# Kernel optimization log

Hardware: AMD Instinct MI355X
Metric: run time of the kernel (lower is better)

The kernel has to match this reference:

```python
import jax, jax.numpy as jnp
import numpy as np

TAU = 0.2        # temperature
LAM = 0.5        # lambda_weight
P = 128          # proj_dim


def l2n(x):
    # tf.math.l2_normalize semantics: x / sqrt(max(sum(x^2), eps))
    return x / jnp.sqrt(jnp.maximum(jnp.sum(x * x, axis=-1, keepdims=True), 1e-12))


def global_head(feat, W1, b1, W2, b2):
    # GlobalAveragePooling2D -> Dense(2048, relu) -> Dense(128); dropout is identity in eval
    g = jnp.mean(feat, axis=(1, 2))                       # [B, C]
    return jax.nn.relu(g @ W1 + b1) @ W2 + b2             # [B, 128]


def dense_head(feat, W1, b1, W2, b2):
    # 1x1 Conv2D(2048, relu) -> 1x1 Conv2D(128) == per-pixel matmuls
    h = jax.nn.relu(jnp.einsum('bhwc,cd->bhwd', feat, W1) + b1)
    return jnp.einsum('bhwd,de->bhwe', h, W2) + b2        # [B, H, W, 128]


def dense_correspondence(q, k):
    b, h, w, c = q.shape
    f1 = q.reshape(b, h * w, c)
    f2 = k.reshape(b, h * w, c)
    sim = jnp.einsum('bnc,bmc->bnm', f1, f2)              # [B, hw, hw]
    idx = jnp.argmax(sim, axis=-1)                        # [B, hw]
    return jnp.take_along_axis(f2, idx[:, :, None], axis=1)  # batched gather


def info_nce(q, k):
    logits = (q @ k.T) / TAU                              # [N, N]
    lse = jax.nn.logsumexp(logits, axis=-1)
    pos = jnp.diagonal(logits)                            # labels = arange(N)
    return jnp.mean(lse - pos)


def queue_info_nce(q, k, queue):
    l_pos = jnp.sum(q * k, axis=-1, keepdims=True)        # [B, 1]
    l_neg = q @ queue.T                                   # [B, Q]
    logits = jnp.concatenate([l_pos, l_neg], axis=1) / TAU
    # labels are all zero -> positive logit is column 0
    return jnp.mean(jax.nn.logsumexp(logits, axis=-1) - logits[:, 0])


def setup_inputs() -> dict:
    key = jax.random.key(0)
    ks = jax.random.split(key, 16)
    B, H, W, C, D = 8, 28, 28, 1024, 2048
    Q = 65536
    s1 = 0.02
    inp = {
        'feat_q': jax.random.normal(ks[0], (B, H, W, C), jnp.float32),
        'feat_k': jax.random.normal(ks[1], (B, H, W, C), jnp.float32),
        'Wg1': jax.random.normal(ks[2], (C, D), jnp.float32) * s1,
        'bg1': jnp.zeros((D,), jnp.float32),
        'Wg2': jax.random.normal(ks[3], (D, P), jnp.float32) * s1,
        'bg2': jnp.zeros((P,), jnp.float32),
        'Wd1': jax.random.normal(ks[4], (C, D), jnp.float32) * s1,
        'bd1': jnp.zeros((D,), jnp.float32),
        'Wd2': jax.random.normal(ks[5], (D, P), jnp.float32) * s1,
        'bd2': jnp.zeros((P,), jnp.float32),
        'mWg1': jax.random.normal(ks[6], (C, D), jnp.float32) * s1,
        'mbg1': jnp.zeros((D,), jnp.float32),
        'mWg2': jax.random.normal(ks[7], (D, P), jnp.float32) * s1,
        'mbg2': jnp.zeros((P,), jnp.float32),
        'mWd1': jax.random.normal(ks[8], (C, D), jnp.float32) * s1,
        'mbd1': jnp.zeros((D,), jnp.float32),
        'mWd2': jax.random.normal(ks[9], (D, P), jnp.float32) * s1,
        'mbd2': jnp.zeros((P,), jnp.float32),
        'queue': l2n(jax.random.normal(ks[10], (Q, P), jnp.float32)),
    }
    return inp


def reference(feat_q, feat_k, Wg1, bg1, Wg2, bg2, Wd1, bd1, Wd2, bd2,
              mWg1, mbg1, mWg2, mbg2, mWd1, mbd1, mWd2, mbd2, queue):
    # student branch
    q_g = l2n(global_head(feat_q, Wg1, bg1, Wg2, bg2))
    q_d = l2n(dense_head(feat_q, Wd1, bd1, Wd2, bd2))
    # momentum (teacher) branch, stop-gradient as in train_step
    k_g = jax.lax.stop_gradient(l2n(global_head(feat_k, mWg1, mbg1, mWg2, mbg2)))
    k_d = jax.lax.stop_gradient(l2n(dense_head(feat_k, mWd1, mbd1, mWd2, mbd2)))
    # post-warmup path (warmup_epochs=0)
    l_g = queue_info_nce(q_g, k_g, queue)
    matched_k = dense_correspondence(q_d, k_d)
    l_d = info_nce(q_d.reshape(-1, P), matched_k.reshape(-1, P))
    total = (1.0 - LAM) * l_g + LAM * l_d
    return total
```

## Files before the change

kernel.cpp:

```cpp
#include <hip/hip_runtime.h>
#include <cstdint>

#define TAU_INV 5.0f
#define L2E 1.4426950408889634f

using ushort = unsigned short;
typedef __attribute__((ext_vector_type(8))) short s16x8;
typedef __attribute__((ext_vector_type(4))) float f32x4;

static __device__ __forceinline__ ushort f2bf(float x) {
  unsigned u = __float_as_uint(x);
  return (ushort)((u + 0x7fffu + ((u >> 16) & 1u)) >> 16);
}

static __device__ __forceinline__ float fexp2(float x) {
#if __has_builtin(__builtin_amdgcn_exp2f)
  return __builtin_amdgcn_exp2f(x);
#else
  return exp2f(x);
#endif
}

static __device__ __forceinline__ void gload_lds16(const void* g, void* l) {
  __builtin_amdgcn_global_load_lds(
      reinterpret_cast<const __attribute__((address_space(1))) void*>(
          reinterpret_cast<uintptr_t>(g)),
      reinterpret_cast<__attribute__((address_space(3))) void*>(
          (unsigned)reinterpret_cast<uintptr_t>(l)),
      16, 0, 0);
}

static __device__ __forceinline__ void xcd_swizzle(int gx, int gy, int& bx, int& by) {
  int nwg = gx * gy;
  int flat = by * gx + bx;
  int q = nwg >> 3, r = nwg & 7;
  int xcd = flat & 7, sl = flat >> 3;
  int tile = (xcd < r ? xcd * (q + 1) : r * (q + 1) + (xcd - r) * q) + sl;
  by = tile / gx;
  bx = tile - by * gx;
}

__global__ void k_prep(const float* __restrict__ fq, const float* __restrict__ fk,
                       ushort* __restrict__ obf, float* __restrict__ gpart,
                       const float* __restrict__ Wd1, const float* __restrict__ mWd1,
                       const float* __restrict__ Wd2, const float* __restrict__ mWd2,
                       ushort* __restrict__ Wt1, ushort* __restrict__ Wt2) {
  int bid = blockIdx.x;
  if (bid < 1792) {
    int pc = bid % 112, yy = bid / 112;
    int br = yy >> 3, b = yy & 7, t = threadIdx.x;
    const float* feat = br ? fk : fq;
    const float* fp = feat + ((size_t)b * 784 + (size_t)pc * 7) * 1024;
    ushort* op = obf + (size_t)br * 6422528 + ((size_t)b * 784 + (size_t)pc * 7) * 1024;
    float4 acc = {0.f, 0.f, 0.f, 0.f};
#pragma unroll
    for (int p = 0; p < 7; ++p) {
      float4 v = ((const float4*)(fp + (size_t)p * 1024))[t];
      acc.x += v.x; acc.y += v.y; acc.z += v.z; acc.w += v.w;
      ushort4 r;
      r.x = f2bf(v.x); r.y = f2bf(v.y); r.z = f2bf(v.z); r.w = f2bf(v.w);
      ((ushort4*)(op + (size_t)p * 1024))[t] = r;
    }
    ((float4*)(gpart + ((size_t)yy * 112 + pc) * 1024))[t] = acc;
  } else {
    int fl2 = bid - 1792;
    int z = fl2 / 2304, fl = fl2 % 2304;
    const float* W;
    ushort* o;
    int bx, by, K, N;
    if (fl < 2048) {
      W = z ? mWd1 : Wd1;
      o = Wt1 + (size_t)z * 2097152;
      bx = fl & 63; by = fl >> 6; K = 1024; N = 2048;
    } else {
      fl -= 2048;
      W = z ? mWd2 : Wd2;
      o = Wt2 + (size_t)z * 262144;
      bx = fl & 3; by = fl >> 2; K = 2048; N = 128;
    }
    __shared__ float tile[32][33];
    int n0 = bx * 32, k0 = by * 32;
    int tx = threadIdx.x & 31, ty = threadIdx.x >> 5;
#pragma unroll
    for (int i = 0; i < 32; i += 8)
      tile[ty + i][tx] = W[(size_t)(k0 + ty + i) * N + n0 + tx];
    __syncthreads();
#pragma unroll
    for (int i = 0; i < 32; i += 8)
      o[(size_t)(n0 + ty + i) * K + k0 + tx] = f2bf(tile[tx][ty + i]);
  }
}

__global__ void k_gpool_fin(const float* __restrict__ gpart, float* __restrict__ g) {
  int idx = blockIdx.x * 256 + threadIdx.x;
  int bb = idx >> 10, c = idx & 1023;
  float s = 0.f;
#pragma unroll 4
  for (int pc = 0; pc < 112; ++pc) s += gpart[((size_t)bb * 112 + pc) * 1024 + c];
  g[idx] = s * (1.0f / 784.0f);
}

__global__ void k_dense1_part(const float* __restrict__ g, const float* __restrict__ W0,
                              const float* __restrict__ W1, float* __restrict__ part1) {
  int br = blockIdx.z;
  const float* gb = g + (size_t)br * 8192;
  const float* W = br ? W1 : W0;
  float* p1 = part1 + (size_t)br * 262144;
  int d = blockIdx.x * 256 + threadIdx.x;
  int k0 = blockIdx.y * 64;
  __shared__ float gs[512];
  for (int i = threadIdx.x; i < 512; i += 256) gs[i] = gb[(i >> 6) * 1024 + k0 + (i & 63)];
  __syncthreads();
  float acc[8] = {};
  for (int kk = 0; kk < 64; ++kk) {
    float w = W[(size_t)(k0 + kk) * 2048 + d];
#pragma unroll
    for (int b = 0; b < 8; ++b) acc[b] += gs[b * 64 + kk] * w;
  }
#pragma unroll
  for (int b = 0; b < 8; ++b) p1[((size_t)blockIdx.y * 8 + b) * 2048 + d] = acc[b];
}

__global__ void k_d12(const float* __restrict__ part1, const float* __restrict__ b10,
                      const float* __restrict__ b11, const float* __restrict__ W20,
                      const float* __restrict__ W21, float* __restrict__ part2) {
  int br = blockIdx.y, k0 = blockIdx.x * 64;
  const float* p1 = part1 + (size_t)br * 262144;
  const float* b1 = br ? b11 : b10;
  const float* W2 = br ? W21 : W20;
  float* p2 = part2 + (size_t)br * 32768;
  __shared__ float hs[512];
  for (int i = threadIdx.x; i < 512; i += 128) {
    int b = i >> 6, kk = i & 63;
    float s = b1[k0 + kk];
#pragma unroll
    for (int ks = 0; ks < 16; ++ks) s += p1[((size_t)ks * 8 + b) * 2048 + k0 + kk];
    hs[i] = fmaxf(s, 0.f);
  }
  __syncthreads();
  int d = threadIdx.x;
  float acc[8] = {};
  for (int kk = 0; kk < 64; ++kk) {
    float w = W2[(size_t)(k0 + kk) * 128 + d];
#pragma unroll
    for (int b = 0; b < 8; ++b) acc[b] += hs[b * 64 + kk] * w;
  }
#pragma unroll
  for (int b = 0; b < 8; ++b) p2[((size_t)blockIdx.x * 8 + b) * 128 + d] = acc[b];
}

__global__ void k_head_fin(const float* __restrict__ p2q, const float* __restrict__ p2k,
                           const float* __restrict__ bq, const float* __restrict__ bk,
                           float* __restrict__ qg, float* __restrict__ kg,
                           float* __restrict__ lpos) {
  int b = blockIdx.x, lane = threadIdx.x;
  float q0 = bq[lane], q1 = bq[lane + 64];
  float k0 = bk[lane], k1 = bk[lane + 64];
#pragma unroll
  for (int s = 0; s < 32; ++s) {
    size_t base = ((size_t)s * 8 + b) * 128;
    q0 += p2q[base + lane]; q1 += p2q[base + lane + 64];
    k0 += p2k[base + lane]; k1 += p2k[base + lane + 64];
  }
  float sq = q0 * q0 + q1 * q1, sk = k0 * k0 + k1 * k1;
#pragma unroll
  for (int d = 1; d < 64; d <<= 1) { sq += __shfl_xor(sq, d); sk += __shfl_xor(sk, d); }
  float rq = 1.0f / sqrtf(fmaxf(sq, 1e-12f));
  float rk = 1.0f / sqrtf(fmaxf(sk, 1e-12f));
  q0 *= rq; q1 *= rq; k0 *= rk; k1 *= rk;
  qg[b * 128 + lane] = q0; qg[b * 128 + 64 + lane] = q1;
  kg[b * 128 + lane] = k0; kg[b * 128 + 64 + lane] = k1;
  float lp = q0 * k0 + q1 * k1;
#pragma unroll
  for (int d = 1; d < 64; d <<= 1) lp += __shfl_xor(lp, d);
  if (lane == 0) lpos[b] = lp;
}

__global__ __launch_bounds__(256) void k_gemm_e1(
    const ushort* __restrict__ A, long sA, const ushort* __restrict__ B, long sB,
    const float* __restrict__ bias0, const float* __restrict__ bias1,
    ushort* __restrict__ O, long sO, int K, int ldOut) {
  __shared__ unsigned char smem[65536];
  const int tid = threadIdx.x;
  int bx = blockIdx.x, by = blockIdx.y;
  const int bz = blockIdx.z;
  xcd_swizzle(gridDim.x, gridDim.y, bx, by);
  const ushort* Ab = A + (size_t)bz * sA;
  const ushort* Bb = B + (size_t)bz * sB;
  const float* bias = bz ? bias1 : bias0;
  ushort* Ob = O + (size_t)bz * sO;
  const int mBase = by * 128, nBase = bx * 128;
  const int lane = tid & 63;
  const int wid = tid >> 6;
  const int wid_u = __builtin_amdgcn_readfirstlane(wid);
  const int wm = wid >> 1, wn = wid & 1;
  const int lg = lane >> 4, li = lane & 15;
  const int lrow = lane >> 3, lchunk = lane & 7;

  const ushort* aSrc[4];
  const ushort* bSrc[4];
  int ldsOff[4];
#pragma unroll
  for (int j = 0; j < 4; ++j) {
    int r = wid_u * 32 + j * 8 + lrow;
    int gc = (lchunk ^ lrow) << 3;
    aSrc[j] = Ab + (size_t)(mBase + r) * K + gc;
    bSrc[j] = Bb + (size_t)(nBase + r) * K + gc;
    ldsOff[j] = (wid_u * 32 + j * 8) * 128;
  }
  f32x4 acc[4][4] = {};

  auto STAGE = [&](int buf, int k0) {
    unsigned base = (unsigned)buf * 32768u;
#pragma unroll
    for (int j = 0; j < 4; ++j) {
      gload_lds16(aSrc[j] + k0, smem + base + ldsOff[j]);
      gload_lds16(bSrc[j] + k0, smem + base + 16384 + ldsOff[j]);
    }
  };

  const int nt = K >> 6;
  STAGE(0, 0);
  __syncthreads();
  for (int t = 0; t < nt; ++t) {
    if (t + 1 < nt) STAGE((t + 1) & 1, (t + 1) << 6);
    const unsigned char* As = smem + (t & 1) * 32768;
    const unsigned char* Bs = As + 16384;
#pragma unroll
    for (int ks = 0; ks < 2; ++ks) {
      s16x8 af[4], bfr[4];
#pragma unroll
      for (int mi = 0; mi < 4; ++mi) {
        int r = wm * 64 + mi * 16 + li;
        af[mi] = *(const s16x8*)(const void*)(As + r * 128 + ((ks * 64 + lg * 16) ^ ((r & 7) << 4)));
      }
#pragma unroll
      for (int ni = 0; ni < 4; ++ni) {
        int c = wn * 64 + ni * 16 + li;
        bfr[ni] = *(const s16x8*)(const void*)(Bs + c * 128 + ((ks * 64 + lg * 16) ^ ((c & 7) << 4)));
      }
#pragma unroll
      for (int mi = 0; mi < 4; ++mi)
#pragma unroll
        for (int ni = 0; ni < 4; ++ni)
          acc[mi][ni] = __builtin_amdgcn_mfma_f32_16x16x32_bf16(af[mi], bfr[ni], acc[mi][ni], 0, 0, 0);
    }
    __syncthreads();
  }

#pragma unroll
  for (int ni = 0; ni < 4; ++ni) {
    int c = nBase + wn * 64 + ni * 16 + li;
    float bv = bias[c];
#pragma unroll
    for (int mi = 0; mi < 4; ++mi) {
#pragma unroll
      for (int rg = 0; rg < 4; ++rg) {
        int r = mBase + wm * 64 + mi * 16 + lg * 4 + rg;
        float v = fmaxf(acc[mi][ni][rg] + bv, 0.f);
        Ob[(size_t)r * ldOut + c] = f2bf(v);
      }
    }
  }
}

__global__ __launch_bounds__(256) void k_gemm_e2(
    const ushort* __restrict__ A, const ushort* __restrict__ B, float* __restrict__ o0,
    int Kloop, int lda, int ldb, long sA, long sB) {
  __shared__ unsigned char smem[65536];
  const int tid = threadIdx.x;
  int bx = blockIdx.x, by = blockIdx.y;
  const int bz = blockIdx.z;
  xcd_swizzle(gridDim.x, gridDim.y, bx, by);
  const ushort* Ab = A + (size_t)(bz >> 2) * sA + (size_t)(bz & 3) * Kloop;
  const ushort* Bb = B + (size_t)(bz >> 2) * sB + (size_t)(bz & 3) * Kloop;
  const int mBase = by * 128, nBase = bx * 128;
  const int lane = tid & 63;
  const int wid = tid >> 6;
  const int wid_u = __builtin_amdgcn_readfirstlane(wid);
  const int wm = wid >> 1, wn = wid & 1;
  const int lg = lane >> 4, li = lane & 15;
  const int lrow = lane >> 3, lchunk = lane & 7;

  const ushort* aSrc[4];
  const ushort* bSrc[4];
  int ldsOff[4];
#pragma unroll
  for (int j = 0; j < 4; ++j) {
    int r = wid_u * 32 + j * 8 + lrow;
    int gc = (lchunk ^ lrow) << 3;
    aSrc[j] = Ab + (size_t)(mBase + r) * lda + gc;
    bSrc[j] = Bb + (size_t)(nBase + r) * ldb + gc;
    ldsOff[j] = (wid_u * 32 + j * 8) * 128;
  }
  f32x4 acc[4][4] = {};

  auto STAGE = [&](int buf, int k0) {
    unsigned base = (unsigned)buf * 32768u;
#pragma unroll
    for (int j = 0; j < 4; ++j) {
      gload_lds16(aSrc[j] + k0, smem + base + ldsOff[j]);
      gload_lds16(bSrc[j] + k0, smem + base + 16384 + ldsOff[j]);
    }
  };

  const int nt = Kloop >> 6;
  STAGE(0, 0);
  __syncthreads();
  for (int t = 0; t < nt; ++t) {
    if (t + 1 < nt) STAGE((t + 1) & 1, (t + 1) << 6);
    const unsigned char* As = smem + (t & 1) * 32768;
    const unsigned char* Bs = As + 16384;
#pragma unroll
    for (int ks = 0; ks < 2; ++ks) {
      s16x8 af[4], bfr[4];
#pragma unroll
      for (int mi = 0; mi < 4; ++mi) {
        int r = wm * 64 + mi * 16 + li;
        af[mi] = *(const s16x8*)(const void*)(As + r * 128 + ((ks * 64 + lg * 16) ^ ((r & 7) << 4)));
      }
#pragma unroll
      for (int ni = 0; ni < 4; ++ni) {
        int c = wn * 64 + ni * 16 + li;
        bfr[ni] = *(const s16x8*)(const void*)(Bs + c * 128 + ((ks * 64 + lg * 16) ^ ((c & 7) << 4)));
      }
#pragma unroll
      for (int mi = 0; mi < 4; ++mi)
#pragma unroll
        for (int ni = 0; ni < 4; ++ni)
          acc[mi][ni] = __builtin_amdgcn_mfma_f32_16x16x32_bf16(af[mi], bfr[ni], acc[mi][ni], 0, 0, 0);
    }
    __syncthreads();
  }

#pragma unroll
  for (int ni = 0; ni < 4; ++ni) {
    int c = nBase + wn * 64 + ni * 16 + li;
#pragma unroll
    for (int mi = 0; mi < 4; ++mi)
#pragma unroll
      for (int rg = 0; rg < 4; ++rg) {
        int r = mBase + wm * 64 + mi * 16 + lg * 4 + rg;
        o0[(size_t)bz * 802816 + (size_t)r * 128 + c] = acc[mi][ni][rg];
      }
  }
}

template <int EPI>
__global__ __launch_bounds__(256) void k_gemm_k128(
    const ushort* __restrict__ A, const ushort* __restrict__ B,
    float* __restrict__ o0, int* __restrict__ o1,
    int Mvalid, int Nvalid, int ntiles, float scale, long sA, long sB) {
  __shared__ unsigned char smem[2048];
  const int tid = threadIdx.x;
  int bx = blockIdx.x, by = blockIdx.y;
  const int bz = blockIdx.z;
  xcd_swizzle(gridDim.x, gridDim.y, bx, by);
  const ushort* Ab = A + (size_t)bz * sA;
  const ushort* Bb = B + (size_t)bz * sB;
  const int mBase = by * 128, nBase = bx * 128;
  const int lane = tid & 63;
  const int wid = tid >> 6;
  const int wm = wid >> 1, wn = wid & 1;
  const int lg = lane >> 4, li = lane & 15;

  const ushort* aRow[4];
  const ushort* bCol[4];
#pragma unroll
  for (int mi = 0; mi < 4; ++mi) {
    int r = mBase + wm * 64 + mi * 16 + li;
    r = r < Mvalid ? r : Mvalid - 1;
    aRow[mi] = Ab + (size_t)r * 128 + lg * 8;
  }
#pragma unroll
  for (int ni = 0; ni < 4; ++ni) {
    int c = nBase + wn * 64 + ni * 16 + li;
    c = c < Nvalid ? c : Nvalid - 1;
    bCol[ni] = Bb + (size_t)c * 128 + lg * 8;
  }

  f32x4 acc[4][4] = {};
#pragma unroll
  for (int ks = 0; ks < 4; ++ks) {
    s16x8 af[4], bfr[4];
#pragma unroll
    for (int mi = 0; mi < 4; ++mi)
      af[mi] = *(const s16x8*)(const void*)(aRow[mi] + ks * 32);
#pragma unroll
    for (int ni = 0; ni < 4; ++ni)
      bfr[ni] = *(const s16x8*)(const void*)(bCol[ni] + ks * 32);
#pragma unroll
    for (int mi = 0; mi < 4; ++mi)
#pragma unroll
      for (int ni = 0; ni < 4; ++ni)
        acc[mi][ni] = __builtin_amdgcn_mfma_f32_16x16x32_bf16(af[mi], bfr[ni], acc[mi][ni], 0, 0, 0);
  }

  if constexpr (EPI == 2) {
    float* reds = (float*)(void*)smem;
#pragma unroll
    for (int mi = 0; mi < 4; ++mi)
#pragma unroll
      for (int rg = 0; rg < 4; ++rg) {
        float s = fexp2(acc[mi][0][rg] * scale) + fexp2(acc[mi][1][rg] * scale) +
                  fexp2(acc[mi][2][rg] * scale) + fexp2(acc[mi][3][rg] * scale);
#pragma unroll
        for (int d = 1; d < 16; d <<= 1) s += __shfl_xor(s, d);
        int rl = wm * 64 + mi * 16 + lg * 4 + rg;
        if (li == 0) reds[rl * 2 + wn] = s;
      }
    __syncthreads();
    if (tid < 128) {
      size_t idx = (size_t)(mBase + tid) * ntiles + bx;
      o0[idx] = reds[tid * 2] + reds[tid * 2 + 1];
    }
  } else {
    float* redv = (float*)(void*)smem;
    int* redi = (int*)(void*)(smem + 1024);
#pragma unroll
    for (int mi = 0; mi < 4; ++mi)
#pragma unroll
      for (int rg = 0; rg < 4; ++rg) {
        float bv = -3.4e38f;
        int bi = 0x7fffffff;
#pragma unroll
        for (int ni = 0; ni < 4; ++ni) {
          int c = nBase + wn * 64 + ni * 16 + li;
          float v = (c < Nvalid) ? acc[mi][ni][rg] : -3.4e38f;
          if (v > bv || (v == bv && c < bi)) { bv = v; bi = c; }
        }
#pragma unroll
        for (int d = 1; d < 16; d <<= 1) {
          float ov = __shfl_xor(bv, d);
          int oi = __shfl_xor(bi, d);
          if (ov > bv || (ov == bv && oi < bi)) { bv = ov; bi = oi; }
        }
        int rl = wm * 64 + mi * 16 + lg * 4 + rg;
        if (li == 0) { redv[rl * 2 + wn] = bv; redi[rl * 2 + wn] = bi; }
      }
    __syncthreads();
    if (tid < 128) {
      int r = mBase + tid;
      if (r < Mvalid) {
        float v0 = redv[tid * 2], v1 = redv[tid * 2 + 1];
        int i0 = redi[tid * 2], i1 = redi[tid * 2 + 1];
        float v = v0; int bi2 = i0;
        if (v1 > v || (v1 == v && i1 < bi2)) { v = v1; bi2 = i1; }
        size_t idx = (size_t)(bz * Mvalid + r) * ntiles + bx;
        o0[idx] = v;
        o1[idx] = bi2;
      }
    }
  }
}

__global__ void k_l2n_rows(const float* __restrict__ part, const float* __restrict__ bias0,
                           const float* __restrict__ bias1, float* __restrict__ of,
                           ushort* __restrict__ ob) {
  int br = blockIdx.y;
  const float* p = part + (size_t)br * 3211264;
  const float* bias = br ? bias1 : bias0;
  float* o = of + (size_t)br * 802816;
  ushort* o2 = ob + (size_t)br * 802816;
  int row = blockIdx.x * 4 + (threadIdx.x >> 6);
  int lane = threadIdx.x & 63;
  size_t i0 = (size_t)row * 128 + lane;
  const size_t SL = 802816;
  float v0 = bias[lane]      + p[i0]      + p[SL + i0]      + p[2 * SL + i0]      + p[3 * SL + i0];
  float v1 = bias[lane + 64] + p[i0 + 64] + p[SL + i0 + 64] + p[2 * SL + i0 + 64] + p[3 * SL + i0 + 64];
  float ss = v0 * v0 + v1 * v1;
#pragma unroll
  for (int d = 1; d < 64; d <<= 1) ss += __shfl_xor(ss, d);
  float r = 1.0f / sqrtf(fmaxf(ss, 1e-12f));
  o[i0] = v0 * r;
  o[i0 + 64] = v1 * r;
  o2[i0] = f2bf(v0 * r);
  o2[i0 + 64] = f2bf(v1 * r);
}

__global__ void k_argmax_gather(const float* __restrict__ pval, const int* __restrict__ pidx,
                                const ushort* __restrict__ kd_bf, ushort* __restrict__ matched_bf,
                                int* __restrict__ idxf) {
  int n = blockIdx.x;
  int b = n / 784;
  float bv = pval[(size_t)n * 7];
  int bi = pidx[(size_t)n * 7];
#pragma unroll
  for (int t = 1; t < 7; ++t) {
    float v = pval[(size_t)n * 7 + t];
    int i2 = pidx[(size_t)n * 7 + t];
    if (v > bv) { bv = v; bi = i2; }
  }
  int lane = threadIdx.x;
  if (lane == 0) idxf[n] = bi;
  const ushort* src = kd_bf + (size_t)(b * 784 + bi) * 128;
  ushort* dst = matched_bf + (size_t)n * 128;
  dst[lane] = src[lane];
  dst[lane + 64] = src[lane + 64];
}

__global__ __launch_bounds__(256) void k_qrow(const float* __restrict__ queue,
                                              const float* __restrict__ qg,
                                              float* __restrict__ ps,
                                              const float* __restrict__ psum,
                                              const int* __restrict__ idxf,
                                              const float* __restrict__ qd,
                                              const float* __restrict__ kd,
                                              float* __restrict__ diff) {
  __shared__ float qs[1024];
  __shared__ float lssum[8][4];
  int tid = threadIdx.x;
  int lane = tid & 63, w = tid >> 6;
  if (blockIdx.x < 256) {
    for (int i = tid; i < 1024; i += 256) qs[i] = qg[i];
    __syncthreads();
    int r = blockIdx.x * 256 + tid;
    const float* qr = queue + (size_t)r * 128;
    float a[8] = {0, 0, 0, 0, 0, 0, 0, 0};
    for (int j = 0; j < 128; j += 4) {
      float4 v = *(const float4*)(const void*)(qr + j);
#pragma unroll
      for (int b = 0; b < 8; ++b)
        a[b] += v.x * qs[b * 128 + j] + v.y * qs[b * 128 + j + 1] +
                v.z * qs[b * 128 + j + 2] + v.w * qs[b * 128 + j + 3];
    }
#pragma unroll
    for (int b = 0; b < 8; ++b) {
      float s = fexp2(a[b] * (TAU_INV * L2E));
#pragma unroll
      for (int d = 1; d < 64; d <<= 1) s += __shfl_xor(s, d);
      if (lane == 0) lssum[b][w] = s;
    }
    __syncthreads();
    if (tid < 8) {
      int b = tid;
      ps[blockIdx.x * 8 + b] = lssum[b][0] + lssum[b][1] + lssum[b][2] + lssum[b][3];
    }
  } else {
    int n = (blockIdx.x - 256) * 4 + w;
    float s = (lane < 49) ? psum[(size_t)n * 49 + lane] : 0.f;
#pragma unroll
    for (int d = 1; d < 64; d <<= 1) s += __shfl_xor(s, d);
    int b = n / 784;
    int mr = b * 784 + idxf[n];
    float pos = qd[(size_t)n * 128 + lane] * kd[(size_t)mr * 128 + lane] +
                qd[(size_t)n * 128 + 64 + lane] * kd[(size_t)mr * 128 + 64 + lane];
#pragma unroll
    for (int d = 1; d < 64; d <<= 1) pos += __shfl_xor(pos, d);
    if (lane == 0) diff[n] = logf(s) - pos * TAU_INV;
  }
}

__global__ void k_final(const float* __restrict__ ps, const float* __restrict__ lpos,
                        const float* __restrict__ diff, float* __restrict__ out) {
  int tid = threadIdx.x;
  int lane = tid & 63, w = tid >> 6;
  __shared__ float sm[4];
  float lg = 0.f;
  for (int b = 0; b < 8; ++b) {
    float s = ps[tid * 8 + b];
#pragma unroll
    for (int d = 1; d < 64; d <<= 1) s += __shfl_xor(s, d);
    if (lane == 0) sm[w] = s;
    __syncthreads();
    if (tid == 0) {
      float S = sm[0] + sm[1] + sm[2] + sm[3];
      float lp = lpos[b] * TAU_INV;
      S += fexp2(lp * L2E);
      lg += logf(S) - lp;
    }
    __syncthreads();
  }
  float v = 0.f;
  for (int i = tid; i < 6272; i += 256) v += diff[i];
#pragma unroll
  for (int d = 1; d < 64; d <<= 1) v += __shfl_xor(v, d);
  if (lane == 0) sm[w] = v;
  __syncthreads();
  if (tid == 0) {
    float ld = sm[0] + sm[1] + sm[2] + sm[3];
    out[0] = 0.5f * (lg * 0.125f) + 0.5f * (ld * (1.0f / 6272.0f));
  }
}

extern "C" void kernel_launch(void* const* d_in, const int* in_sizes, int n_in,
                              void* d_out, int out_size, void* d_ws, size_t ws_size,
                              hipStream_t stream) {
  (void)in_sizes; (void)n_in; (void)out_size; (void)ws_size;
  const float* feat_q = (const float*)d_in[0];
  const float* feat_k = (const float*)d_in[1];
  const float* Wg1 = (const float*)d_in[2];
  const float* bg1 = (const float*)d_in[3];
  const float* Wg2 = (const float*)d_in[4];
  const float* bg2 = (const float*)d_in[5];
  const float* Wd1 = (const float*)d_in[6];
  const float* bd1 = (const float*)d_in[7];
  const float* Wd2 = (const float*)d_in[8];
  const float* bd2 = (const float*)d_in[9];
  const float* mWg1 = (const float*)d_in[10];
  const float* mbg1 = (const float*)d_in[11];
  const float* mWg2 = (const float*)d_in[12];
  const float* mbg2 = (const float*)d_in[13];
  const float* mWd1 = (const float*)d_in[14];
  const float* mbd1 = (const float*)d_in[15];
  const float* mWd2 = (const float*)d_in[16];
  const float* mbd2 = (const float*)d_in[17];
  const float* queue = (const float*)d_in[18];
  float* out = (float*)d_out;

  char* ws = (char*)d_ws;
  size_t off = 0;
  auto alloc = [&](size_t bytes) -> void* {
    void* p = (void*)(ws + off);
    off += (bytes + 255) & ~(size_t)255;
    return p;
  };

  ushort* feat_bf = (ushort*)alloc(2ull * 6272 * 1024 * 2);
  ushort* Wd1t2 = (ushort*)alloc(2ull * 2048 * 1024 * 2);
  ushort* Wd2t2 = (ushort*)alloc(2ull * 128 * 2048 * 2);
  ushort* h_bf2 = (ushort*)alloc(2ull * 6272 * 2048 * 2);
  float* e2part2 = (float*)alloc(2ull * 4 * 6272 * 128 * 4);
  float* qdkd = (float*)alloc(2ull * 6272 * 128 * 4);
  ushort* qdkd_bf = (ushort*)alloc(2ull * 6272 * 128 * 2);
  ushort* matched_bf = (ushort*)alloc(6272ull * 128 * 2);
  float* psum = (float*)alloc(6272ull * 49 * 4);
  float* pval = (float*)alloc(6272ull * 7 * 4);
  int* pidx = (int*)alloc(6272ull * 7 * 4);
  int* idxf = (int*)alloc(6272ull * 4);
  float* gpart = (float*)alloc(16ull * 112 * 1024 * 4);
  float* g2 = (float*)alloc(2ull * 8 * 1024 * 4);
  float* part1 = (float*)alloc(2ull * 16 * 8 * 2048 * 4);
  float* part2 = (float*)alloc(2ull * 32 * 8 * 128 * 4);
  float* qg = (float*)alloc(8ull * 128 * 4);
  float* kg = (float*)alloc(8ull * 128 * 4);
  float* l_pos = (float*)alloc(8ull * 4);
  float* qpart_s = (float*)alloc(256ull * 8 * 4);
  float* diff = (float*)alloc(6272ull * 4);

  k_prep<<<6400, 256, 0, stream>>>(feat_q, feat_k, feat_bf, gpart,
                                   Wd1, mWd1, Wd2, mWd2, Wd1t2, Wd2t2);
  k_gpool_fin<<<64, 256, 0, stream>>>(gpart, g2);

  k_dense1_part<<<dim3(8, 16, 2), 256, 0, stream>>>(g2, Wg1, mWg1, part1);
  k_d12<<<dim3(32, 2), 128, 0, stream>>>(part1, bg1, mbg1, Wg2, mWg2, part2);
  k_head_fin<<<8, 64, 0, stream>>>(part2, part2 + 32768, bg2, mbg2, qg, kg, l_pos);

  k_gemm_e1<<<dim3(16, 49, 2), 256, 0, stream>>>(feat_bf, 6422528, Wd1t2, 2097152,
                                                 bd1, mbd1, h_bf2, 12845056, 1024, 2048);
  k_gemm_e2<<<dim3(1, 49, 8), 256, 0, stream>>>(h_bf2, Wd2t2, e2part2,
                                                512, 2048, 2048, 12845056, 262144);
  k_l2n_rows<<<dim3(1568, 2), 256, 0, stream>>>(e2part2, bd2, mbd2, qdkd, qdkd_bf);

  k_gemm_k128<3><<<dim3(7, 7, 8), 256, 0, stream>>>(qdkd_bf, qdkd_bf + 802816, pval, pidx,
                                                    784, 784, 7, 0.f, 784l * 128, 784l * 128);
  k_argmax_gather<<<6272, 64, 0, stream>>>(pval, pidx, qdkd_bf + 802816, matched_bf, idxf);

  k_gemm_k128<2><<<dim3(49, 49, 1), 256, 0, stream>>>(qdkd_bf, matched_bf, psum, nullptr,
                                                      6272, 6272, 49, TAU_INV * L2E, 0, 0);

  k_qrow<<<1824, 256, 0, stream>>>(queue, qg, qpart_s, psum, idxf, qdkd, qdkd + 802816, diff);
  k_final<<<1, 256, 0, stream>>>(qpart_s, l_pos, diff, out);
}
```

Measured before the change: 234.0 us.

## Fold global-head kernels into dense GEMM launches as extra grid slices

Removes four small global-head launches (pool finish, dense1, dense2, head finalize) by embedding their work as extra z-slices or an extra block in the dense-branch GEMM and L2-normalize kernels. The pooling reduction is folded into the dense1 blocks, each of which now recomputes the pooled means for its k-slice. This cuts launch overhead and serialization of tiny kernels, letting the global head overlap with the large GEMMs. The cost is redundant pooling reads across d-chunks and wasted early-exit blocks in the padded grids.

New measurement: 289.1 us. 1.24x slower.

```diff
diff --git a/kernel.cpp b/kernel.cpp
--- a/kernel.cpp
+++ b/kernel.cpp
@@ -91,99 +91,44 @@
   }
 }
 
-__global__ void k_gpool_fin(const float* __restrict__ gpart, float* __restrict__ g) {
-  int idx = blockIdx.x * 256 + threadIdx.x;
-  int bb = idx >> 10, c = idx & 1023;
-  float s = 0.f;
-#pragma unroll 4
-  for (int pc = 0; pc < 112; ++pc) s += gpart[((size_t)bb * 112 + pc) * 1024 + c];
-  g[idx] = s * (1.0f / 784.0f);
-}
-
-__global__ void k_dense1_part(const float* __restrict__ g, const float* __restrict__ W0,
-                              const float* __restrict__ W1, float* __restrict__ part1) {
-  int br = blockIdx.z;
-  const float* gb = g + (size_t)br * 8192;
-  const float* W = br ? W1 : W0;
-  float* p1 = part1 + (size_t)br * 262144;
-  int d = blockIdx.x * 256 + threadIdx.x;
-  int k0 = blockIdx.y * 64;
-  __shared__ float gs[512];
-  for (int i = threadIdx.x; i < 512; i += 256) gs[i] = gb[(i >> 6) * 1024 + k0 + (i & 63)];
-  __syncthreads();
-  float acc[8] = {};
-  for (int kk = 0; kk < 64; ++kk) {
-    float w = W[(size_t)(k0 + kk) * 2048 + d];
-#pragma unroll
-    for (int b = 0; b < 8; ++b) acc[b] += gs[b * 64 + kk] * w;
-  }
-#pragma unroll
-  for (int b = 0; b < 8; ++b) p1[((size_t)blockIdx.y * 8 + b) * 2048 + d] = acc[b];
-}
-
-__global__ void k_d12(const float* __restrict__ part1, const float* __restrict__ b10,
-                      const float* __restrict__ b11, const float* __restrict__ W20,
-                      const float* __restrict__ W21, float* __restrict__ part2) {
-  int br = blockIdx.y, k0 = blockIdx.x * 64;
-  const float* p1 = part1 + (size_t)br * 262144;
-  const float* b1 = br ? b11 : b10;
-  const float* W2 = br ? W21 : W20;
-  float* p2 = part2 + (size_t)br * 32768;
-  __shared__ float hs[512];
-  for (int i = threadIdx.x; i < 512; i += 128) {
-    int b = i >> 6, kk = i & 63;
-    float s = b1[k0 + kk];
-#pragma unroll
-    for (int ks = 0; ks < 16; ++ks) s += p1[((size_t)ks * 8 + b) * 2048 + k0 + kk];
-    hs[i] = fmaxf(s, 0.f);
-  }
-  __syncthreads();
-  int d = threadIdx.x;
-  float acc[8] = {};
-  for (int kk = 0; kk < 64; ++kk) {
-    float w = W2[(size_t)(k0 + kk) * 128 + d];
-#pragma unroll
-    for (int b = 0; b < 8; ++b) acc[b] += hs[b * 64 + kk] * w;
-  }
-#pragma unroll
-  for (int b = 0; b < 8; ++b) p2[((size_t)blockIdx.x * 8 + b) * 128 + d] = acc[b];
-}
-
-__global__ void k_head_fin(const float* __restrict__ p2q, const float* __restrict__ p2k,
-                           const float* __restrict__ bq, const float* __restrict__ bk,
-                           float* __restrict__ qg, float* __restrict__ kg,
-                           float* __restrict__ lpos) {
-  int b = blockIdx.x, lane = threadIdx.x;
-  float q0 = bq[lane], q1 = bq[lane + 64];
-  float k0 = bk[lane], k1 = bk[lane + 64];
-#pragma unroll
-  for (int s = 0; s < 32; ++s) {
-    size_t base = ((size_t)s * 8 + b) * 128;
-    q0 += p2q[base + lane]; q1 += p2q[base + lane + 64];
-    k0 += p2k[base + lane]; k1 += p2k[base + lane + 64];
-  }
-  float sq = q0 * q0 + q1 * q1, sk = k0 * k0 + k1 * k1;
-#pragma unroll
-  for (int d = 1; d < 64; d <<= 1) { sq += __shfl_xor(sq, d); sk += __shfl_xor(sk, d); }
-  float rq = 1.0f / sqrtf(fmaxf(sq, 1e-12f));
-  float rk = 1.0f / sqrtf(fmaxf(sk, 1e-12f));
-  q0 *= rq; q1 *= rq; k0 *= rk; k1 *= rk;
-  qg[b * 128 + lane] = q0; qg[b * 128 + 64 + lane] = q1;
-  kg[b * 128 + lane] = k0; kg[b * 128 + 64 + lane] = k1;
-  float lp = q0 * k0 + q1 * k1;
-#pragma unroll
-  for (int d = 1; d < 64; d <<= 1) lp += __shfl_xor(lp, d);
-  if (lane == 0) lpos[b] = lp;
-}
-
-__global__ __launch_bounds__(256) void k_gemm_e1(
+__global__ __launch_bounds__(256) void k_e1d1(
     const ushort* __restrict__ A, long sA, const ushort* __restrict__ B, long sB,
     const float* __restrict__ bias0, const float* __restrict__ bias1,
-    ushort* __restrict__ O, long sO, int K, int ldOut) {
+    ushort* __restrict__ O, long sO, int K, int ldOut,
+    const float* __restrict__ gpart, const float* __restrict__ Wg1,
+    const float* __restrict__ mWg1, float* __restrict__ part1) {
   __shared__ unsigned char smem[65536];
   const int tid = threadIdx.x;
+  const int bz = blockIdx.z;
+  if (bz == 2) {
+    int flat = blockIdx.y * 16 + blockIdx.x;
+    if (flat >= 256) return;
+    int dchunk = flat & 7, kslice = (flat >> 3) & 15, br = flat >> 7;
+    const float* gp = gpart + (size_t)br * 917504;
+    const float* W = br ? mWg1 : Wg1;
+    float* p1 = part1 + (size_t)br * 262144;
+    int d = dchunk * 256 + tid;
+    int k0 = kslice * 64;
+    float* gs = (float*)(void*)smem;
+    for (int i = tid; i < 512; i += 256) {
+      int b = i >> 6, kk = i & 63;
+      float s = 0.f;
+#pragma unroll 4
+      for (int pc = 0; pc < 112; ++pc) s += gp[((size_t)(b * 112 + pc)) * 1024 + k0 + kk];
+      gs[i] = s * (1.0f / 784.0f);
+    }
+    __syncthreads();
+    float acc[8] = {};
+    for (int kk = 0; kk < 64; ++kk) {
+      float w = W[(size_t)(k0 + kk) * 2048 + d];
+#pragma unroll
+      for (int b = 0; b < 8; ++b) acc[b] += gs[b * 64 + kk] * w;
+    }
+#pragma unroll
+    for (int b = 0; b < 8; ++b) p1[((size_t)kslice * 8 + b) * 2048 + d] = acc[b];
+    return;
+  }
   int bx = blockIdx.x, by = blockIdx.y;
-  const int bz = blockIdx.z;
   xcd_swizzle(gridDim.x, gridDim.y, bx, by);
   const ushort* Ab = A + (size_t)bz * sA;
   const ushort* Bb = B + (size_t)bz * sB;
@@ -264,13 +209,44 @@
   }
 }
 
-__global__ __launch_bounds__(256) void k_gemm_e2(
+__global__ __launch_bounds__(256) void k_e2d12(
     const ushort* __restrict__ A, const ushort* __restrict__ B, float* __restrict__ o0,
-    int Kloop, int lda, int ldb, long sA, long sB) {
+    int Kloop, int lda, int ldb, long sA, long sB,
+    const float* __restrict__ part1, const float* __restrict__ b10,
+    const float* __restrict__ b11, const float* __restrict__ W20,
+    const float* __restrict__ W21, float* __restrict__ part2) {
   __shared__ unsigned char smem[65536];
   const int tid = threadIdx.x;
+  const int bz = blockIdx.z;
+  if (bz == 8) {
+    int by2 = blockIdx.y;
+    if (by2 >= 32) return;
+    int k0 = by2 * 64;
+    int half = tid >> 7, d = tid & 127;
+    float* hs = (float*)(void*)smem + half * 512;
+    const float* p1 = part1 + (size_t)half * 262144;
+    const float* b1 = half ? b11 : b10;
+    const float* W2 = half ? W21 : W20;
+    float* p2 = part2 + (size_t)half * 32768;
+    for (int i = d; i < 512; i += 128) {
+      int b = i >> 6, kk = i & 63;
+      float s = b1[k0 + kk];
+#pragma unroll
+      for (int ks = 0; ks < 16; ++ks) s += p1[((size_t)ks * 8 + b) * 2048 + k0 + kk];
+      hs[i] = fmaxf(s, 0.f);
+    }
+    __syncthreads();
+    float acc[8] = {};
+    for (int kk = 0; kk < 64; ++kk) {
+      float w = W2[(size_t)(k0 + kk) * 128 + d];
+#pragma unroll
+      for (int b = 0; b < 8; ++b) acc[b] += hs[b * 64 + kk] * w;
+    }
+#pragma unroll
+    for (int b = 0; b < 8; ++b) p2[((size_t)by2 * 8 + b) * 128 + d] = acc[b];
+    return;
+  }
   int bx = blockIdx.x, by = blockIdx.y;
-  const int bz = blockIdx.z;
   xcd_swizzle(gridDim.x, gridDim.y, bx, by);
   const ushort* Ab = A + (size_t)(bz >> 2) * sA + (size_t)(bz & 3) * Kloop;
   const ushort* Bb = B + (size_t)(bz >> 2) * sB + (size_t)(bz & 3) * Kloop;
@@ -344,6 +320,60 @@
         o0[(size_t)bz * 802816 + (size_t)r * 128 + c] = acc[mi][ni][rg];
       }
   }
+}
+
+__global__ void k_l2nhf(const float* __restrict__ part, const float* __restrict__ bias0,
+                        const float* __restrict__ bias1, float* __restrict__ of,
+                        ushort* __restrict__ ob,
+                        const float* __restrict__ p2q, const float* __restrict__ p2k,
+                        const float* __restrict__ bq, const float* __restrict__ bk,
+                        float* __restrict__ qg, float* __restrict__ kg,
+                        float* __restrict__ lpos) {
+  int lane = threadIdx.x & 63, w = threadIdx.x >> 6;
+  if (blockIdx.x == 1568) {
+    if (blockIdx.y) return;
+    for (int b = w; b < 8; b += 4) {
+      float q0 = bq[lane], q1 = bq[lane + 64];
+      float k0 = bk[lane], k1 = bk[lane + 64];
+#pragma unroll
+      for (int s = 0; s < 32; ++s) {
+        size_t base = ((size_t)s * 8 + b) * 128;
+        q0 += p2q[base + lane]; q1 += p2q[base + lane + 64];
+        k0 += p2k[base + lane]; k1 += p2k[base + lane + 64];
+      }
+      float sq = q0 * q0 + q1 * q1, sk = k0 * k0 + k1 * k1;
+#pragma unroll
+      for (int d = 1; d < 64; d <<= 1) { sq += __shfl_xor(sq, d); sk += __shfl_xor(sk, d); }
+      float rq = 1.0f / sqrtf(fmaxf(sq, 1e-12f));
+      float rk = 1.0f / sqrtf(fmaxf(sk, 1e-12f));
+      q0 *= rq; q1 *= rq; k0 *= rk; k1 *= rk;
+      qg[b * 128 + lane] = q0; qg[b * 128 + 64 + lane] = q1;
+      kg[b * 128 + lane] = k0; kg[b * 128 + 64 + lane] = k1;
+      float lp = q0 * k0 + q1 * k1;
+#pragma unroll
+      for (int d = 1; d < 64; d <<= 1) lp += __shfl_xor(lp, d);
+      if (lane == 0) lpos[b] = lp;
+    }
+    return;
+  }
+  int br = blockIdx.y;
+  const float* p = part + (size_t)br * 3211264;
+  const float* bias = br ? bias1 : bias0;
+  float* o = of + (size_t)br * 802816;
+  ushort* o2 = ob + (size_t)br * 802816;
+  int row = blockIdx.x * 4 + w;
+  size_t i0 = (size_t)row * 128 + lane;
+  const size_t SL = 802816;
+  float v0 = bias[lane]      + p[i0]      + p[SL + i0]      + p[2 * SL + i0]      + p[3 * SL + i0];
+  float v1 = bias[lane + 64] + p[i0 + 64] + p[SL + i0 + 64] + p[2 * SL + i0 + 64] + p[3 * SL + i0 + 64];
+  float ss = v0 * v0 + v1 * v1;
+#pragma unroll
+  for (int d = 1; d < 64; d <<= 1) ss += __shfl_xor(ss, d);
+  float r = 1.0f / sqrtf(fmaxf(ss, 1e-12f));
+  o[i0] = v0 * r;
+  o[i0 + 64] = v1 * r;
+  o2[i0] = f2bf(v0 * r);
+  o2[i0 + 64] = f2bf(v1 * r);
 }
 
 template <int EPI>
@@ -452,30 +482,6 @@
       }
     }
   }
-}
-
-__global__ void k_l2n_rows(const float* __restrict__ part, const float* __restrict__ bias0,
-                           const float* __restrict__ bias1, float* __restrict__ of,
-                           ushort* __restrict__ ob) {
-  int br = blockIdx.y;
-  const float* p = part + (size_t)br * 3211264;
-  const float* bias = br ? bias1 : bias0;
-  float* o = of + (size_t)br * 802816;
-  ushort* o2 = ob + (size_t)br * 802816;
-  int row = blockIdx.x * 4 + (threadIdx.x >> 6);
-  int lane = threadIdx.x & 63;
-  size_t i0 = (size_t)row * 128 + lane;
-  const size_t SL = 802816;
-  float v0 = bias[lane]      + p[i0]      + p[SL + i0]      + p[2 * SL + i0]      + p[3 * SL + i0];
-  float v1 = bias[lane + 64] + p[i0 + 64] + p[SL + i0 + 64] + p[2 * SL + i0 + 64] + p[3 * SL + i0 + 64];
-  float ss = v0 * v0 + v1 * v1;
-#pragma unroll
-  for (int d = 1; d < 64; d <<= 1) ss += __shfl_xor(ss, d);
-  float r = 1.0f / sqrtf(fmaxf(ss, 1e-12f));
-  o[i0] = v0 * r;
-  o[i0 + 64] = v1 * r;
-  o2[i0] = f2bf(v0 * r);
-  o2[i0 + 64] = f2bf(v1 * r);
 }
 
 __global__ void k_argmax_gather(const float* __restrict__ pval, const int* __restrict__ pidx,
@@ -629,7 +635,6 @@
   int* pidx = (int*)alloc(6272ull * 7 * 4);
   int* idxf = (int*)alloc(6272ull * 4);
   float* gpart = (float*)alloc(16ull * 112 * 1024 * 4);
-  float* g2 = (float*)alloc(2ull * 8 * 1024 * 4);
   float* part1 = (float*)alloc(2ull * 16 * 8 * 2048 * 4);
   float* part2 = (float*)alloc(2ull * 32 * 8 * 128 * 4);
   float* qg = (float*)alloc(8ull * 128 * 4);
@@ -640,17 +645,17 @@
 
   k_prep<<<6400, 256, 0, stream>>>(feat_q, feat_k, feat_bf, gpart,
                                    Wd1, mWd1, Wd2, mWd2, Wd1t2, Wd2t2);
-  k_gpool_fin<<<64, 256, 0, stream>>>(gpart, g2);
-
-  k_dense1_part<<<dim3(8, 16, 2), 256, 0, stream>>>(g2, Wg1, mWg1, part1);
-  k_d12<<<dim3(32, 2), 128, 0, stream>>>(part1, bg1, mbg1, Wg2, mWg2, part2);
-  k_head_fin<<<8, 64, 0, stream>>>(part2, part2 + 32768, bg2, mbg2, qg, kg, l_pos);
-
-  k_gemm_e1<<<dim3(16, 49, 2), 256, 0, stream>>>(feat_bf, 6422528, Wd1t2, 2097152,
-                                                 bd1, mbd1, h_bf2, 12845056, 1024, 2048);
-  k_gemm_e2<<<dim3(1, 49, 8), 256, 0, stream>>>(h_bf2, Wd2t2, e2part2,
-                                                512, 2048, 2048, 12845056, 262144);
-  k_l2n_rows<<<dim3(1568, 2), 256, 0, stream>>>(e2part2, bd2, mbd2, qdkd, qdkd_bf);
+
+  k_e1d1<<<dim3(16, 49, 3), 256, 0, stream>>>(feat_bf, 6422528, Wd1t2, 2097152,
+                                              bd1, mbd1, h_bf2, 12845056, 1024, 2048,
+                                              gpart, Wg1, mWg1, part1);
+
+  k_e2d12<<<dim3(1, 49, 9), 256, 0, stream>>>(h_bf2, Wd2t2, e2part2,
+                                              512, 2048, 2048, 12845056, 262144,
+                                              part1, bg1, mbg1, Wg2, mWg2, part2);
+
+  k_l2nhf<<<dim3(1569, 2), 256, 0, stream>>>(e2part2, bd2, mbd2, qdkd, qdkd_bf,
+                                             part2, part2 + 32768, bg2, mbg2, qg, kg, l_pos);
 
   k_gemm_k128<3><<<dim3(7, 7, 8), 256, 0, stream>>>(qdkd_bf, qdkd_bf + 802816, pval, pidx,
                                                     784, 784, 7, 0.f, 784l * 128, 784l * 128);
```
